# Optimization experiments

Hardware: AMD Instinct MI355X
Metric: run time of the kernel (lower is better)

Reference implementation:

```python
import jax, jax.numpy as jnp
import numpy as np

N = 8192        # nodes
V = 50000       # vocab = len(dict_node_names)
EMB = 256       # embedding_dim
XI = EMB // 2   # x_increased_dim = 128
DIN = EMB + XI  # 384, SelfAtt_ dim
H = 4           # n_heads
D = 128         # WGAT output_dim per head (fusion dim)
E = 131072      # edges
CHUNK = 32768   # chunk_size (E % CHUNK == 0)


def _ln(x, g, b, eps=1e-5):
    m = jnp.mean(x, axis=-1, keepdims=True)
    v = jnp.mean((x - m) ** 2, axis=-1, keepdims=True)
    return (x - m) * jax.lax.rsqrt(v + eps) * g + b


def _wgat(emb, src, dst, edge_attr, wi, bi, wj, bj, wt, bt, attn):
    # x_i = features at destination (aggregation target), x_j = source/neighbor
    x_i = emb[dst]                                   # [E, din]
    x_j = emb[src]                                   # [E, din]
    h = (x_i @ wi + bi).reshape(E, H, D) + (x_j @ wj + bj).reshape(E, H, D)
    a = jnp.einsum('ehd,hd->eh', h, attn)            # [E, H]
    a = a * edge_attr[:, None]                       # edge weights pre-softmax
    # faithful chunked softmax: normalize over edges WITHIN each chunk (dim=0 per chunk)
    a = jax.nn.softmax(a.reshape(E // CHUNK, CHUNK, H), axis=1).reshape(E, H)
    xt = (x_j @ wt + bt).reshape(E, H, D)            # [E, H, D]
    msg = jnp.einsum('ehd,eh->ed', xt, a)            # sum over heads -> [E, D]
    return jax.ops.segment_sum(msg, dst, num_segments=N)  # aggr='add'


def _emb_forward(ids, edge_index, x, edge_attr, embed,
                 qkv_w, qkv_b, proj_w, proj_b, fuse_w, fuse_b, ln1_g, ln1_b,
                 wi0, bi0, wj0, bj0, wt0, bt0, attn0, skip0_w, skip0_b,
                 wi1, bi1, wj1, bj1, wt1, bt1, attn1, skip1_w, skip1_b,
                 ln2_g, ln2_b):
    E_i = embed[ids]                                 # [N, EMB] gather
    z = jnp.concatenate([jnp.tile(x, (1, XI)), E_i], axis=-1)   # [N, DIN]
    # SelfAtt_ : full N x N attention over nodes, scale = DIN**-0.5
    qkv = z @ qkv_w + qkv_b
    q, k, v = jnp.split(qkv, 3, axis=-1)
    att = jax.nn.softmax((q @ k.T) * (DIN ** -0.5), axis=-1) @ v
    z = att @ proj_w + proj_b                        # [N, DIN]
    emb = jax.nn.silu(_ln(z @ fuse_w + fuse_b, ln1_g, ln1_b)) + E_i  # [N, EMB]
    src, dst = edge_index[0], edge_index[1]
    emb = _wgat(emb, src, dst, edge_attr, wi0, bi0, wj0, bj0, wt0, bt0, attn0)  # [N, D]
    s0 = emb @ skip0_w + skip0_b
    emb = _wgat(emb, src, dst, edge_attr, wi1, bi1, wj1, bj1, wt1, bt1, attn1)  # [N, D]
    s1 = emb @ skip1_w + skip1_b
    emb = _ln(emb + (s0 + s1) * 0.5, ln2_g, ln2_b)
    return emb


def setup_inputs() -> dict:
    key = jax.random.key(0)
    ks = jax.random.split(key, 32)

    def w(k, shape, scale=0.05):
        return jax.random.normal(k, shape, jnp.float32) * scale

    inp = {}
    inp['ids'] = jax.random.randint(ks[0], (N,), 0, V)
    inp['x'] = jax.random.normal(ks[1], (N, 1), jnp.float32)
    inp['edge_attr'] = jax.random.uniform(ks[2], (E,), jnp.float32)
    inp['edge_index'] = jax.random.randint(ks[3], (2, E), 0, N)
    inp['embed'] = w(ks[4], (V, EMB), 1.0)
    inp['qkv_w'] = w(ks[5], (DIN, 3 * DIN)); inp['qkv_b'] = jnp.zeros((3 * DIN,), jnp.float32)
    inp['proj_w'] = w(ks[6], (DIN, DIN));    inp['proj_b'] = jnp.zeros((DIN,), jnp.float32)
    inp['fuse_w'] = w(ks[7], (DIN, EMB));    inp['fuse_b'] = jnp.zeros((EMB,), jnp.float32)
    inp['ln1_g'] = jnp.ones((EMB,), jnp.float32); inp['ln1_b'] = jnp.zeros((EMB,), jnp.float32)
    # WGAT layer 0: in=EMB, out=D per head, H heads
    inp['wi0'] = w(ks[8], (EMB, H * D));  inp['bi0'] = jnp.zeros((H * D,), jnp.float32)
    inp['wj0'] = w(ks[9], (EMB, H * D));  inp['bj0'] = jnp.zeros((H * D,), jnp.float32)
    inp['wt0'] = w(ks[10], (EMB, H * D)); inp['bt0'] = jnp.zeros((H * D,), jnp.float32)
    inp['attn0'] = w(ks[11], (H, D), 0.1)
    inp['skip0_w'] = w(ks[12], (D, D));   inp['skip0_b'] = jnp.zeros((D,), jnp.float32)
    # WGAT layer 1: in=D
    inp['wi1'] = w(ks[13], (D, H * D));   inp['bi1'] = jnp.zeros((H * D,), jnp.float32)
    inp['wj1'] = w(ks[14], (D, H * D));   inp['bj1'] = jnp.zeros((H * D,), jnp.float32)
    inp['wt1'] = w(ks[15], (D, H * D));   inp['bt1'] = jnp.zeros((H * D,), jnp.float32)
    inp['attn1'] = w(ks[16], (H, D), 0.1)
    inp['skip1_w'] = w(ks[17], (D, D));   inp['skip1_b'] = jnp.zeros((D,), jnp.float32)
    inp['ln2_g'] = jnp.ones((D,), jnp.float32); inp['ln2_b'] = jnp.zeros((D,), jnp.float32)
    return inp


def reference(ids, x, edge_attr, edge_index, embed,
              qkv_w, qkv_b, proj_w, proj_b, fuse_w, fuse_b, ln1_g, ln1_b,
              wi0, bi0, wj0, bj0, wt0, bt0, attn0, skip0_w, skip0_b,
              wi1, bi1, wj1, bj1, wt1, bt1, attn1, skip1_w, skip1_b,
              ln2_g, ln2_b):
    emb = _emb_forward(ids, edge_index, x, edge_attr, embed,
                       qkv_w, qkv_b, proj_w, proj_b, fuse_w, fuse_b, ln1_g, ln1_b,
                       wi0, bi0, wj0, bj0, wt0, bt0, attn0, skip0_w, skip0_b,
                       wi1, bi1, wj1, bj1, wt1, bt1, attn1, skip1_w, skip1_b,
                       ln2_g, ln2_b)
    return (emb, embed, ids)
```

## Files before the change

### kernel.cpp

```cpp
#include <hip/hip_runtime.h>

typedef __attribute__((ext_vector_type(8))) short bfrag;
typedef __attribute__((ext_vector_type(4))) float f4;

#define MFMA(a,b,c) __builtin_amdgcn_mfma_f32_16x16x32_bf16(a,b,c,0,0,0)

__device__ __forceinline__ unsigned short f2b(float x){
  union { float f; unsigned int u; } v; v.f = x;
  unsigned int r = v.u + 0x7fffu + ((v.u >> 16) & 1u);
  return (unsigned short)(r >> 16);
}
__device__ __forceinline__ float b2f(unsigned short h){
  union { unsigned int u; float f; } v; v.u = ((unsigned int)h) << 16;
  return v.f;
}

__global__ __launch_bounds__(256) void k_prep(
    const float* __restrict__ qkv_w, const float* __restrict__ proj_w,
    const float* __restrict__ fuse_w, const float* __restrict__ wt0,
    const float* __restrict__ wt1, const float* __restrict__ sk0w,
    const float* __restrict__ wi0, const float* __restrict__ bi0,
    const float* __restrict__ wj0, const float* __restrict__ bj0,
    const float* __restrict__ wi1, const float* __restrict__ bi1,
    const float* __restrict__ wj1, const float* __restrict__ bj1,
    const float* __restrict__ attn0, const float* __restrict__ attn1,
    const float* __restrict__ bt0, const float* __restrict__ bt1,
    const float* __restrict__ sk0b,
    const float* __restrict__ embed, const int* __restrict__ ids,
    unsigned short* __restrict__ BtQKV, unsigned short* __restrict__ BtPROJ,
    unsigned short* __restrict__ BtFUSE, unsigned short* __restrict__ BtT0,
    unsigned short* __restrict__ BtT1,
    float* __restrict__ biasT0, float* __restrict__ biasT1,
    float* __restrict__ wsum, float* __restrict__ Ei)
{
  int b = blockIdx.x, t = threadIdx.x;
  if (b < 1152) {
    int idx = b*256 + t; int k = idx/1152, n = idx - k*1152;
    BtQKV[(size_t)n*256 + k] = f2b(qkv_w[128*1152 + idx]);
  } else if (b < 1728) {
    int idx = (b-1152)*256 + t; int k = idx/384, n = idx - k*384;
    BtPROJ[(size_t)n*384 + k] = f2b(proj_w[idx]);
  } else if (b < 2112) {
    int idx = (b-1728)*256 + t; int k = idx/256, n = idx - k*256;
    BtFUSE[(size_t)n*384 + k] = f2b(fuse_w[idx]);
  } else if (b < 2624) {
    int idx = (b-2112)*256 + t; int k = idx/512, n = idx - k*512;
    BtT0[(size_t)n*256 + k] = f2b(wt0[idx]);
  } else if (b < 2880) {
    int idx = (b-2624)*256 + t; int k = idx/512, n = idx - k*512;
    BtT1[(size_t)n*128 + k] = f2b(wt1[idx]);
  } else if (b < 2944) {
    int idx = (b-2880)*256 + t; int k = idx/128, n = idx - k*128;
    BtT1[(size_t)(512+n)*128 + k] = f2b(sk0w[idx]);
  } else if (b < 2948) {
    int idx = (b-2944)*256 + t;
    int h = idx >> 8, k = idx & 255;
    float s = 0.f;
    for (int d = 0; d < 128; ++d) s += wi0[(size_t)k*512 + h*128 + d] * attn0[h*128 + d];
    BtT0[(size_t)(512 + h)*256 + k] = f2b(s);
    if (idx < 4) {
      float sb = 0.f;
      for (int d = 0; d < 128; ++d) sb += bi0[idx*128 + d] * attn0[idx*128 + d];
      biasT0[512 + idx] = sb;
    }
  } else if (b < 2952) {
    int idx = (b-2948)*256 + t;
    int h = idx >> 8, k = idx & 255;
    float s = 0.f;
    for (int d = 0; d < 128; ++d) s += wj0[(size_t)k*512 + h*128 + d] * attn0[h*128 + d];
    BtT0[(size_t)(516 + h)*256 + k] = f2b(s);
    if (idx < 4) {
      float sb = 0.f;
      for (int d = 0; d < 128; ++d) sb += bj0[idx*128 + d] * attn0[idx*128 + d];
      biasT0[516 + idx] = sb;
    }
  } else if (b < 2954) {
    int idx = (b-2952)*256 + t;
    int h = idx >> 7, k = idx & 127;
    float s = 0.f;
    for (int d = 0; d < 128; ++d) s += wi1[(size_t)k*512 + h*128 + d] * attn1[h*128 + d];
    BtT1[(size_t)(640 + h)*128 + k] = f2b(s);
    if (idx < 4) {
      float sb = 0.f;
      for (int d = 0; d < 128; ++d) sb += bi1[idx*128 + d] * attn1[idx*128 + d];
      biasT1[640 + idx] = sb;
    }
  } else if (b < 2956) {
    int idx = (b-2954)*256 + t;
    int h = idx >> 7, k = idx & 127;
    float s = 0.f;
    for (int d = 0; d < 128; ++d) s += wj1[(size_t)k*512 + h*128 + d] * attn1[h*128 + d];
    BtT1[(size_t)(644 + h)*128 + k] = f2b(s);
    if (idx < 4) {
      float sb = 0.f;
      for (int d = 0; d < 128; ++d) sb += bj1[idx*128 + d] * attn1[idx*128 + d];
      biasT1[644 + idx] = sb;
    }
  } else if (b < 2958) {
    int idx = (b-2956)*256 + t; biasT0[idx] = bt0[idx];
  } else if (b < 2960) {
    int idx = (b-2958)*256 + t; biasT1[idx] = bt1[idx];
  } else if (b < 2961) {
    if (t < 128) biasT1[512 + t] = sk0b[t];
  } else if (b < 2966) {
    int n = (b-2961)*256 + t;
    if (n < 1152) {
      float s = 0.f;
      for (int k = 0; k < 128; ++k) s += qkv_w[(size_t)k*1152 + n];
      wsum[n] = s;
    }
  } else {
    int idx = (b-2966)*256 + t;
    int n = idx >> 6, c4 = idx & 63;
    reinterpret_cast<float4*>(Ei)[idx] =
        reinterpret_cast<const float4*>(embed + (size_t)ids[n]*256)[c4];
  }
}

__global__ void k_outcopy(const float* __restrict__ embed, const int* __restrict__ ids,
                          float* __restrict__ out){
  int i = blockIdx.x*256 + threadIdx.x;
  if (i < 3200000)
    reinterpret_cast<float4*>(out)[262144 + i] = reinterpret_cast<const float4*>(embed)[i];
  if (i < 8192) out[13848576 + i] = (float)ids[i];
}

__global__ void k_deg(const int* __restrict__ ei, int* __restrict__ deg){
  int e = blockIdx.x*256 + threadIdx.x; if (e >= 131072) return;
  atomicAdd(&deg[ei[131072 + e]], 1);
}

__global__ __launch_bounds__(1024) void k_scan(const int* __restrict__ deg,
                                               int* __restrict__ off, int* __restrict__ cursor){
  int t = threadIdx.x;
  int v[8]; int s = 0;
  #pragma unroll
  for (int i=0;i<8;++i){ v[i] = s; s += deg[t*8 + i]; }
  int lane = t & 63, w = t >> 6;
  int si = s;
  for (int o=1;o<64;o<<=1){ int u = __shfl_up(si, o); if (lane >= o) si += u; }
  __shared__ int wsum[16];
  if (lane == 63) wsum[w] = si;
  __syncthreads();
  if (t < 16) {
    int x = wsum[t];
    for (int o=1;o<16;o<<=1){ int u = __shfl_up(x, o); if (t >= o) x += u; }
    wsum[t] = x;
  }
  __syncthreads();
  int wbase = (w == 0) ? 0 : wsum[w-1];
  int base = wbase + (si - s);
  #pragma unroll
  for (int i=0;i<8;++i){ int o2 = base + v[i]; off[t*8+i] = o2; cursor[t*8+i] = o2; }
  if (t == 1023) off[8192] = wbase + si;
}

__global__ void k_fill(const int* __restrict__ ei, int* __restrict__ cursor,
                       int* __restrict__ elist){
  int e = blockIdx.x*256 + threadIdx.x; if (e >= 131072) return;
  int d = ei[131072 + e];
  int slot = atomicAdd(&cursor[d], 1);
  elist[slot] = e;
}

__global__ __launch_bounds__(256) void k_gemm(
    const float* __restrict__ A, int lda,
    const unsigned short* __restrict__ Bt, int K,
    const float* __restrict__ bias,
    float* __restrict__ C, int ldc, int mode,
    const float* __restrict__ xv, const float* __restrict__ wsum,
    unsigned short* __restrict__ qO, unsigned short* __restrict__ kO,
    unsigned short* __restrict__ vO)
{
  __shared__ unsigned short As[128*40];
  __shared__ unsigned short Bs[128*40];
  const int t = threadIdx.x;
  const int wid = t >> 6, l = t & 63;
  const int lr = l & 15, lg = l >> 4;
  const int arow0 = blockIdx.y*128, bn0 = blockIdx.x*128;
  const int wr = (wid >> 1)*64, wc = (wid & 1)*64;
  f4 zero = {0.f,0.f,0.f,0.f};
  f4 acc[4][4];
  #pragma unroll
  for (int i=0;i<4;++i)
    #pragma unroll
    for (int j=0;j<4;++j) acc[i][j] = zero;

  for (int k0 = 0; k0 < K; k0 += 32) {
    #pragma unroll
    for (int p=0;p<4;++p) {
      int row = p*32 + (t>>3);
      int c4  = (t&7)*4;
      float4 v = *reinterpret_cast<const float4*>(A + (size_t)(arow0+row)*lda + k0 + c4);
      ushort4 h4;
      h4.x = f2b(v.x); h4.y = f2b(v.y); h4.z = f2b(v.z); h4.w = f2b(v.w);
      *reinterpret_cast<ushort4*>(&As[row*40 + c4]) = h4;
    }
    #pragma unroll
    for (int p=0;p<2;++p) {
      int n  = p*64 + (t>>2);
      int c8 = (t&3)*8;
      int4 v = *reinterpret_cast<const int4*>(Bt + (size_t)(bn0+n)*K + k0 + c8);
      *reinterpret_cast<int4*>(&Bs[n*40 + c8]) = v;
    }
    __syncthreads();
    bfrag af[4], bfm[4];
    #pragma unroll
    for (int mi=0;mi<4;++mi) af[mi] = *reinterpret_cast<const bfrag*>(&As[(wr+mi*16+lr)*40 + lg*8]);
    #pragma unroll
    for (int ni=0;ni<4;++ni) bfm[ni] = *reinterpret_cast<const bfrag*>(&Bs[(wc+ni*16+lr)*40 + lg*8]);
    #pragma unroll
    for (int mi=0;mi<4;++mi)
      #pragma unroll
      for (int ni=0;ni<4;++ni)
        acc[mi][ni] = MFMA(af[mi], bfm[ni], acc[mi][ni]);
    __syncthreads();
  }
  #pragma unroll
  for (int mi=0;mi<4;++mi) {
    #pragma unroll
    for (int ni=0;ni<4;++ni) {
      int col = bn0 + wc + ni*16 + lr;
      float bv = bias[col];
      float wsv = (mode==1) ? wsum[col] : 0.f;
      #pragma unroll
      for (int i=0;i<4;++i) {
        int row = arow0 + wr + mi*16 + lg*4 + i;
        float val = acc[mi][ni][i] + bv;
        if (mode == 1) {
          val += xv[row]*wsv;
          if (col < 384) val *= 0.05103103631f;
          unsigned short hv = f2b(val);
          if (col < 384)      qO[(size_t)row*384 + col] = hv;
          else if (col < 768) kO[(size_t)row*384 + col - 384] = hv;
          else                vO[(size_t)(col-768)*8192 + row] = hv;
        } else {
          C[(size_t)row*ldc + col] = val;
        }
      }
    }
  }
}

__global__ __launch_bounds__(256,2) void k_flash(
    const unsigned short* __restrict__ qg,
    const unsigned short* __restrict__ kg,
    const unsigned short* __restrict__ vg,
    unsigned short* __restrict__ Opart, float* __restrict__ mpart, float* __restrict__ lpart)
{
  __shared__ unsigned short Ks[32*384];
  __shared__ unsigned short Vs[2][384*32];
  __shared__ unsigned short Ps[64*40];
  __shared__ float f_s[64];

  const int t = threadIdx.x;
  const int w = t >> 6, l = t & 63;
  const int lr = l & 15, lg = l >> 4;
  const int qbi = blockIdx.x >> 2, split = blockIdx.x & 3;
  const int qbase = qbi * 64;

  #define STAGE_K(JJ) do { \
    _Pragma("unroll") \
    for (int p_=0;p_<6;++p_) { \
      int idx_ = p_*256 + t; \
      int row_ = idx_ / 48, uu_ = idx_ - row_*48; \
      int ug_ = uu_ ^ (row_ & 7); \
      const unsigned short* gp_ = kg + (size_t)((JJ) + row_)*384 + ug_*8; \
      __builtin_amdgcn_global_load_lds((const __attribute__((address_space(1))) void*)gp_, \
          (__attribute__((address_space(3))) void*)&Ks[idx_*8], 16, 0, 0); \
    } } while(0)

  #define STAGE_V(JJ, BUF) do { \
    _Pragma("unroll") \
    for (int p_=0;p_<6;++p_) { \
      int idx_ = p_*256 + t; \
      int d_ = idx_ >> 2, u_ = idx_ & 3; \
      const unsigned short* gp_ = vg + (size_t)d_*8192 + (JJ) + u_*8; \
      __builtin_amdgcn_global_load_lds((const __attribute__((address_space(1))) void*)gp_, \
          (__attribute__((address_space(3))) void*)&Vs[BUF][idx_*8], 16, 0, 0); \
    } } while(0)

  bfrag qf[12];
  #pragma unroll
  for (int kk=0;kk<12;++kk)
    qf[kk] = *reinterpret_cast<const bfrag*>(qg + (size_t)(qbase + w*16 + lr)*384 + kk*32 + lg*8);

  f4 zero = {0.f,0.f,0.f,0.f};
  f4 o[4][6];
  #pragma unroll
  for (int a=0;a<4;++a)
    #pragma unroll
    for (int b=0;b<6;++b) o[a][b] = zero;

  float m = -3e38f, lsum = 0.f;
  const int j0beg = split*2048, jend = j0beg + 2048;

  STAGE_K(j0beg);
  STAGE_V(j0beg, 0);
  __syncthreads();
  int cur = 0;

  for (int j0 = j0beg; j0 < jend; j0 += 32) {
    f4 s0 = zero, s1 = zero;
    __builtin_amdgcn_s_setprio(1);
    #pragma unroll
    for (int kk=0;kk<12;++kk) {
      int su = ((kk*4 + lg) ^ (lr & 7)) * 8;
      bfrag k0 = *reinterpret_cast<const bfrag*>(&Ks[lr*384 + su]);
      bfrag k1 = *reinterpret_cast<const bfrag*>(&Ks[(16+lr)*384 + su]);
      s0 = MFMA(k0, qf[kk], s0);
      s1 = MFMA(k1, qf[kk], s1);
    }
    __builtin_amdgcn_s_setprio(0);

    float mt = fmaxf(fmaxf(fmaxf(s0[0],s0[1]),fmaxf(s0[2],s0[3])),
                     fmaxf(fmaxf(s1[0],s1[1]),fmaxf(s1[2],s1[3])));
    mt = fmaxf(mt, __shfl_xor(mt,16));
    mt = fmaxf(mt, __shfl_xor(mt,32));
    bool grew = mt > m;
    float mn = grew ? mt : m;
    float p0[4], p1[4];
    float sum = 0.f;
    #pragma unroll
    for (int i=0;i<4;++i) {
      p0[i] = __expf(s0[i]-mn); p1[i] = __expf(s1[i]-mn);
      sum += p0[i] + p1[i];
    }
    sum += __shfl_xor(sum,16);
    sum += __shfl_xor(sum,32);
    float f = 1.f;
    if (__any(grew)) {
      f = __expf(m - mn);
      lsum = lsum * f + sum;
      m = mn;
    } else {
      lsum += sum;
    }

    unsigned int pk0 = (unsigned int)f2b(p0[0]) | ((unsigned int)f2b(p0[1]) << 16);
    unsigned int pk1 = (unsigned int)f2b(p0[2]) | ((unsigned int)f2b(p0[3]) << 16);
    unsigned int pk2 = (unsigned int)f2b(p1[0]) | ((unsigned int)f2b(p1[1]) << 16);
    unsigned int pk3 = (unsigned int)f2b(p1[2]) | ((unsigned int)f2b(p1[3]) << 16);
    int prow = (w*16 + lr)*40;
    *reinterpret_cast<unsigned int*>(&Ps[prow + lg*4])          = pk0;
    *reinterpret_cast<unsigned int*>(&Ps[prow + lg*4 + 2])      = pk1;
    *reinterpret_cast<unsigned int*>(&Ps[prow + 16 + lg*4])     = pk2;
    *reinterpret_cast<unsigned int*>(&Ps[prow + 16 + lg*4 + 2]) = pk3;
    if (lg == 0) f_s[w*16 + lr] = f;

    __syncthreads();

    if (j0 + 32 < jend) { STAGE_K(j0 + 32); STAGE_V(j0 + 32, cur ^ 1); }

    bfrag pf[4], vf[6];
    #pragma unroll
    for (int qt=0;qt<4;++qt)
      pf[qt] = *reinterpret_cast<const bfrag*>(&Ps[(qt*16+lr)*40 + lg*8]);
    #pragma unroll
    for (int dt=0;dt<6;++dt)
      vf[dt] = *reinterpret_cast<const bfrag*>(&Vs[cur][(w*96 + dt*16 + lr)*32 + lg*8]);
    #pragma unroll
    for (int qt=0;qt<4;++qt) {
      #pragma unroll
      for (int i=0;i<4;++i) {
        float fr = f_s[qt*16 + lg*4 + i];
        #pragma unroll
        for (int dt=0;dt<6;++dt) o[qt][dt][i] *= fr;
      }
    }
    __builtin_amdgcn_s_setprio(1);
    #pragma unroll
    for (int qt=0;qt<4;++qt)
      #pragma unroll
      for (int dt=0;dt<6;++dt)
        o[qt][dt] = MFMA(pf[qt], vf[dt], o[qt][dt]);
    __builtin_amdgcn_s_setprio(0);

    __syncthreads();
    cur ^= 1;
  }
  #undef STAGE_K
  #undef STAGE_V

  unsigned short* Op = Opart + (size_t)split*8192*384;
  #pragma unroll
  for (int qt=0;qt<4;++qt)
    #pragma unroll
    for (int dt=0;dt<6;++dt)
      #pragma unroll
      for (int i=0;i<4;++i)
        Op[(size_t)(qbase + qt*16 + lg*4 + i)*384 + w*96 + dt*16 + lr] = f2b(o[qt][dt][i]);
  if (lg == 0) {
    mpart[split*8192 + qbase + w*16 + lr] = m;
    lpart[split*8192 + qbase + w*16 + lr] = lsum;
  }
}

__global__ void k_combine(const unsigned short* __restrict__ Op, const float* __restrict__ mp,
                          const float* __restrict__ lp, float* __restrict__ att)
{
  int gid = blockIdx.x*256 + threadIdx.x;
  int row = gid / 384;
  float m0 = mp[row], m1 = mp[8192+row], m2 = mp[16384+row], m3 = mp[24576+row];
  float M = fmaxf(fmaxf(m0,m1), fmaxf(m2,m3));
  float w0 = __expf(m0-M), w1 = __expf(m1-M), w2 = __expf(m2-M), w3 = __expf(m3-M);
  float L = lp[row]*w0 + lp[8192+row]*w1 + lp[16384+row]*w2 + lp[24576+row]*w3;
  const size_t Z = (size_t)8192*384;
  float acc = b2f(Op[gid])*w0 + b2f(Op[Z+gid])*w1 + b2f(Op[2*Z+gid])*w2 + b2f(Op[3*Z+gid])*w3;
  att[gid] = acc / L;
}

__global__ __launch_bounds__(256) void k_ln1(const float* __restrict__ pre, const float* __restrict__ Ei,
                      const float* __restrict__ g, const float* __restrict__ b,
                      float* __restrict__ out)
{
  int row = blockIdx.x, c = threadIdx.x;
  float v = pre[(size_t)row*256 + c];
  float s1 = v, s2 = v*v;
  #pragma unroll
  for (int o1=32;o1;o1>>=1){ s1 += __shfl_down(s1,o1); s2 += __shfl_down(s2,o1); }
  __shared__ float a1[4], a2[4];
  if ((c&63)==0){ a1[c>>6] = s1; a2[c>>6] = s2; }
  __syncthreads();
  float S1 = a1[0]+a1[1]+a1[2]+a1[3], S2 = a2[0]+a2[1]+a2[2]+a2[3];
  float mean = S1*(1.f/256.f), var = S2*(1.f/256.f) - mean*mean;
  float y = (v-mean)*rsqrtf(var+1e-5f)*g[c] + b[c];
  float sig = 1.f/(1.f+__expf(-y));
  out[(size_t)row*256 + c] = y*sig + Ei[(size_t)row*256 + c];
}

__global__ void k_escore(const int* __restrict__ ei, const float* __restrict__ ea,
                         const float* __restrict__ TC, int ldc, int aoff,
                         float* __restrict__ sc)
{
  int e = blockIdx.x*256 + threadIdx.x; if (e >= 131072) return;
  int s = ei[e], d = ei[131072 + e];
  float wv = ea[e];
  #pragma unroll
  for (int h=0; h<4; ++h) {
    float ai = TC[(size_t)d*ldc + aoff + h];
    float aj = TC[(size_t)s*ldc + aoff + 4 + h];
    sc[e*4 + h] = (ai + aj) * wv;
  }
}

__global__ __launch_bounds__(1024) void k_cstats(const float* __restrict__ sc,
                        float* __restrict__ mx, float* __restrict__ sm)
{
  int ch = blockIdx.x;
  int c = ch >> 2, h = ch & 3;
  int t = threadIdx.x;
  const float* base = sc + (size_t)c*131072 + h;
  float m = -3e38f;
  for (int i=t; i<32768; i+=1024) m = fmaxf(m, base[(size_t)i*4]);
  #pragma unroll
  for (int o1=32;o1;o1>>=1) m = fmaxf(m, __shfl_down(m,o1));
  __shared__ float red[16];
  if ((t&63)==0) red[t>>6] = m;
  __syncthreads();
  if (t == 0) { float x = red[0]; for (int i=1;i<16;++i) x = fmaxf(x, red[i]); red[0] = x; }
  __syncthreads();
  float M = red[0];
  float s = 0.f;
  for (int i=t; i<32768; i+=1024) s += __expf(base[(size_t)i*4] - M);
  #pragma unroll
  for (int o1=32;o1;o1>>=1) s += __shfl_down(s,o1);
  __shared__ float red2[16];
  if ((t&63)==0) red2[t>>6] = s;
  __syncthreads();
  if (t == 0) { float x = 0.f; for (int i=0;i<16;++i) x += red2[i]; mx[ch] = M; sm[ch] = x; }
}

__global__ void k_pnorm(float* __restrict__ sc, const float* __restrict__ mx,
                        const float* __restrict__ sm)
{
  int i = blockIdx.x*256 + threadIdx.x;
  int e = i >> 2, h = i & 3;
  int ch = (e >> 15)*4 + h;
  sc[i] = __expf(sc[i] - mx[ch]) / sm[ch];
}

__global__ __launch_bounds__(128) void k_aggr(const int* __restrict__ off,
                      const int* __restrict__ elist, const int* __restrict__ ei,
                      const float* __restrict__ sc,
                      const float* __restrict__ TC, int ldc, float* __restrict__ g)
{
  int n = blockIdx.x, d = threadIdx.x;
  int qb = off[n], qe = off[n+1];
  float acc = 0.f;
  for (int q = qb; q < qe; ++q) {
    int e = elist[q];
    int s = ei[e];
    float4 p = *reinterpret_cast<const float4*>(&sc[e*4]);
    const float* Tr = TC + (size_t)s*ldc;
    acc += p.x*Tr[d] + p.y*Tr[128+d] + p.z*Tr[256+d] + p.w*Tr[384+d];
  }
  g[(size_t)n*128 + d] = acc;
}

__global__ __launch_bounds__(128) void k_final(const float* __restrict__ g1, const float* __restrict__ TC1,
                       const float* __restrict__ sw, const float* __restrict__ sb,
                       const float* __restrict__ lg2, const float* __restrict__ lb2,
                       float* __restrict__ out)
{
  int row = blockIdx.x, c = threadIdx.x;
  __shared__ float gr[128];
  float gv = g1[(size_t)row*128 + c];
  gr[c] = gv; __syncthreads();
  float s1 = sb[c];
  #pragma unroll 8
  for (int k=0;k<128;++k) s1 += gr[k]*sw[k*128 + c];
  float s0 = TC1[(size_t)row*768 + 512 + c];
  float v = gv + 0.5f*(s0 + s1);
  float m1 = v, m2 = v*v;
  #pragma unroll
  for (int o1=32;o1;o1>>=1){ m1 += __shfl_down(m1,o1); m2 += __shfl_down(m2,o1); }
  __shared__ float a1[2], a2[2];
  if ((c&63)==0){ a1[c>>6]=m1; a2[c>>6]=m2; }
  __syncthreads();
  float S1 = a1[0]+a1[1], S2 = a2[0]+a2[1];
  float mean = S1*(1.f/128.f), var = S2*(1.f/128.f) - mean*mean;
  out[(size_t)row*128 + c] = (v-mean)*rsqrtf(var+1e-5f)*lg2[c] + lb2[c];
}

extern "C" void kernel_launch(void* const* d_in, const int* in_sizes, int n_in,
                              void* d_out, int out_size, void* d_ws, size_t ws_size,
                              hipStream_t stream)
{
  const int*   ids    = (const int*)  d_in[0];
  const float* x      = (const float*)d_in[1];
  const float* ea     = (const float*)d_in[2];
  const int*   eidx   = (const int*)  d_in[3];
  const float* embed  = (const float*)d_in[4];
  const float* qkv_w  = (const float*)d_in[5];
  const float* qkv_b  = (const float*)d_in[6];
  const float* proj_w = (const float*)d_in[7];
  const float* proj_b = (const float*)d_in[8];
  const float* fuse_w = (const float*)d_in[9];
  const float* fuse_b = (const float*)d_in[10];
  const float* ln1_g  = (const float*)d_in[11];
  const float* ln1_b  = (const float*)d_in[12];
  const float* wi0 = (const float*)d_in[13]; const float* bi0 = (const float*)d_in[14];
  const float* wj0 = (const float*)d_in[15]; const float* bj0 = (const float*)d_in[16];
  const float* wt0 = (const float*)d_in[17]; const float* bt0 = (const float*)d_in[18];
  const float* attn0 = (const float*)d_in[19];
  const float* sk0w = (const float*)d_in[20]; const float* sk0b = (const float*)d_in[21];
  const float* wi1 = (const float*)d_in[22]; const float* bi1 = (const float*)d_in[23];
  const float* wj1 = (const float*)d_in[24]; const float* bj1 = (const float*)d_in[25];
  const float* wt1 = (const float*)d_in[26]; const float* bt1 = (const float*)d_in[27];
  const float* attn1 = (const float*)d_in[28];
  const float* sk1w = (const float*)d_in[29]; const float* sk1b = (const float*)d_in[30];
  const float* ln2_g = (const float*)d_in[31]; const float* ln2_b = (const float*)d_in[32];

  char* ws = (char*)d_ws;
  const size_t MBy = (size_t)1 << 20;

  unsigned short* BtQKV  = (unsigned short*)(ws + 0);
  unsigned short* BtPROJ = (unsigned short*)(ws + 589824);
  unsigned short* BtFUSE = (unsigned short*)(ws + 884736);
  unsigned short* BtT0   = (unsigned short*)(ws + 1081344);
  unsigned short* BtT1   = (unsigned short*)(ws + 1409024);
  float* biasT0 = (float*)(ws + 1605632);
  float* biasT1 = (float*)(ws + 1608192);
  float* wsum   = (float*)(ws + 1611264);
  float* mxb    = (float*)(ws + 1615872);
  float* smb    = (float*)(ws + 1615936);
  int* deg    = (int*)(ws + 1703936);
  int* cursor = (int*)(ws + 1736704);
  int* off    = (int*)(ws + 1769472);

  float* Ei   = (float*)(ws + 2*MBy);
  unsigned short* qb = (unsigned short*)(ws + 10*MBy);
  unsigned short* kb = (unsigned short*)(ws + 17*MBy);
  unsigned short* vb = (unsigned short*)(ws + 24*MBy);
  float* att  = (float*)(ws + 31*MBy);
  float* z2   = (float*)(ws + 10*MBy);
  float* pre  = (float*)(ws + 45*MBy);
  float* emb0 = (float*)(ws + 31*MBy);
  float* TC0  = (float*)(ws + 43*MBy);
  float* sc0  = (float*)(ws + 26*MBy);
  float* g0   = (float*)(ws + 2*MBy);
  float* TC1  = (float*)(ws + 6*MBy);
  float* sc1  = (float*)(ws + 43*MBy);
  float* g1   = (float*)(ws + 47448064);
  int* elist  = (int*)(ws + 64*MBy);

  float* out = (float*)d_out;
  unsigned short* Opart = (unsigned short*)d_out;
  float* mpart = out + 6815744;
  float* lpart = out + 6848512;

  hipMemsetAsync(ws, 0, 2*MBy, stream);

  k_prep<<<5014, 256, 0, stream>>>(qkv_w, proj_w, fuse_w, wt0, wt1, sk0w,
                                   wi0, bi0, wj0, bj0, wi1, bi1, wj1, bj1,
                                   attn0, attn1, bt0, bt1, sk0b, embed, ids,
                                   BtQKV, BtPROJ, BtFUSE, BtT0, BtT1,
                                   biasT0, biasT1, wsum, Ei);
  k_deg<<<512, 256, 0, stream>>>(eidx, deg);
  k_scan<<<1, 1024, 0, stream>>>(deg, off, cursor);
  k_fill<<<512, 256, 0, stream>>>(eidx, cursor, elist);

  k_gemm<<<dim3(9,64), 256, 0, stream>>>(Ei, 256, BtQKV, 256, qkv_b, nullptr, 0, 1,
                                         x, wsum, qb, kb, vb);
  k_flash<<<512, 256, 0, stream>>>(qb, kb, vb, Opart, mpart, lpart);
  k_combine<<<12288, 256, 0, stream>>>(Opart, mpart, lpart, att);
  k_outcopy<<<12500, 256, 0, stream>>>(embed, ids, out);

  k_gemm<<<dim3(3,64), 256, 0, stream>>>(att, 384, BtPROJ, 384, proj_b, z2, 384, 0,
                                         nullptr, nullptr, nullptr, nullptr, nullptr);
  k_gemm<<<dim3(2,64), 256, 0, stream>>>(z2, 384, BtFUSE, 384, fuse_b, pre, 256, 0,
                                         nullptr, nullptr, nullptr, nullptr, nullptr);
  k_ln1<<<8192, 256, 0, stream>>>(pre, Ei, ln1_g, ln1_b, emb0);

  k_gemm<<<dim3(5,64), 256, 0, stream>>>(emb0, 256, BtT0, 256, biasT0, TC0, 640, 0,
                                         nullptr, nullptr, nullptr, nullptr, nullptr);
  k_escore<<<512, 256, 0, stream>>>(eidx, ea, TC0, 640, 512, sc0);
  k_cstats<<<16, 1024, 0, stream>>>(sc0, mxb, smb);
  k_pnorm<<<2048, 256, 0, stream>>>(sc0, mxb, smb);
  k_aggr<<<8192, 128, 0, stream>>>(off, elist, eidx, sc0, TC0, 640, g0);

  k_gemm<<<dim3(6,64), 256, 0, stream>>>(g0, 128, BtT1, 128, biasT1, TC1, 768, 0,
                                         nullptr, nullptr, nullptr, nullptr, nullptr);
  k_escore<<<512, 256, 0, stream>>>(eidx, ea, TC1, 768, 640, sc1);
  k_cstats<<<16, 1024, 0, stream>>>(sc1, mxb, smb);
  k_pnorm<<<2048, 256, 0, stream>>>(sc1, mxb, smb);
  k_aggr<<<8192, 128, 0, stream>>>(off, elist, eidx, sc1, TC1, 768, g1);

  k_final<<<8192, 128, 0, stream>>>(g1, TC1, sk1w, sk1b, ln2_g, ln2_b, out);
}
```

Baseline: 474.8 us.

## Fold proj into fuse weights, fuse split-K combine into GEMM, lazy flash rescale

After: 531.3 us. 11.9% more time.

```diff
diff --git a/kernel.cpp b/kernel.cpp
--- a/kernel.cpp
+++ b/kernel.cpp
@@ -17,7 +17,9 @@
 
 __global__ __launch_bounds__(256) void k_prep(
     const float* __restrict__ qkv_w, const float* __restrict__ proj_w,
-    const float* __restrict__ fuse_w, const float* __restrict__ wt0,
+    const float* __restrict__ proj_b, const float* __restrict__ fuse_w,
+    const float* __restrict__ fuse_b,
+    const float* __restrict__ wt0,
     const float* __restrict__ wt1, const float* __restrict__ sk0w,
     const float* __restrict__ wi0, const float* __restrict__ bi0,
     const float* __restrict__ wj0, const float* __restrict__ bj0,
@@ -27,9 +29,9 @@
     const float* __restrict__ bt0, const float* __restrict__ bt1,
     const float* __restrict__ sk0b,
     const float* __restrict__ embed, const int* __restrict__ ids,
-    unsigned short* __restrict__ BtQKV, unsigned short* __restrict__ BtPROJ,
-    unsigned short* __restrict__ BtFUSE, unsigned short* __restrict__ BtT0,
-    unsigned short* __restrict__ BtT1,
+    unsigned short* __restrict__ BtQKV, unsigned short* __restrict__ BtW2,
+    unsigned short* __restrict__ BtT0, unsigned short* __restrict__ BtT1,
+    float* __restrict__ biasW2,
     float* __restrict__ biasT0, float* __restrict__ biasT1,
     float* __restrict__ wsum, float* __restrict__ Ei)
 {
@@ -37,23 +39,26 @@
   if (b < 1152) {
     int idx = b*256 + t; int k = idx/1152, n = idx - k*1152;
     BtQKV[(size_t)n*256 + k] = f2b(qkv_w[128*1152 + idx]);
-  } else if (b < 1728) {
-    int idx = (b-1152)*256 + t; int k = idx/384, n = idx - k*384;
-    BtPROJ[(size_t)n*384 + k] = f2b(proj_w[idx]);
-  } else if (b < 2112) {
-    int idx = (b-1728)*256 + t; int k = idx/256, n = idx - k*256;
-    BtFUSE[(size_t)n*384 + k] = f2b(fuse_w[idx]);
-  } else if (b < 2624) {
-    int idx = (b-2112)*256 + t; int k = idx/512, n = idx - k*512;
+  } else if (b < 1536) {
+    int k = b - 1152;
+    float s = 0.f;
+    for (int j = 0; j < 384; ++j) s += proj_w[(size_t)k*384 + j] * fuse_w[(size_t)j*256 + t];
+    BtW2[(size_t)t*384 + k] = f2b(s);
+  } else if (b == 1536) {
+    float s = fuse_b[t];
+    for (int j = 0; j < 384; ++j) s += proj_b[j] * fuse_w[(size_t)j*256 + t];
+    biasW2[t] = s;
+  } else if (b < 2049) {
+    int idx = (b-1537)*256 + t; int k = idx/512, n = idx - k*512;
     BtT0[(size_t)n*256 + k] = f2b(wt0[idx]);
-  } else if (b < 2880) {
-    int idx = (b-2624)*256 + t; int k = idx/512, n = idx - k*512;
+  } else if (b < 2305) {
+    int idx = (b-2049)*256 + t; int k = idx/512, n = idx - k*512;
     BtT1[(size_t)n*128 + k] = f2b(wt1[idx]);
-  } else if (b < 2944) {
-    int idx = (b-2880)*256 + t; int k = idx/128, n = idx - k*128;
+  } else if (b < 2369) {
+    int idx = (b-2305)*256 + t; int k = idx/128, n = idx - k*128;
     BtT1[(size_t)(512+n)*128 + k] = f2b(sk0w[idx]);
-  } else if (b < 2948) {
-    int idx = (b-2944)*256 + t;
+  } else if (b < 2373) {
+    int idx = (b-2369)*256 + t;
     int h = idx >> 8, k = idx & 255;
     float s = 0.f;
     for (int d = 0; d < 128; ++d) s += wi0[(size_t)k*512 + h*128 + d] * attn0[h*128 + d];
@@ -63,8 +68,8 @@
       for (int d = 0; d < 128; ++d) sb += bi0[idx*128 + d] * attn0[idx*128 + d];
       biasT0[512 + idx] = sb;
     }
-  } else if (b < 2952) {
-    int idx = (b-2948)*256 + t;
+  } else if (b < 2377) {
+    int idx = (b-2373)*256 + t;
     int h = idx >> 8, k = idx & 255;
     float s = 0.f;
     for (int d = 0; d < 128; ++d) s += wj0[(size_t)k*512 + h*128 + d] * attn0[h*128 + d];
@@ -74,8 +79,8 @@
       for (int d = 0; d < 128; ++d) sb += bj0[idx*128 + d] * attn0[idx*128 + d];
       biasT0[516 + idx] = sb;
     }
-  } else if (b < 2954) {
-    int idx = (b-2952)*256 + t;
+  } else if (b < 2379) {
+    int idx = (b-2377)*256 + t;
     int h = idx >> 7, k = idx & 127;
     float s = 0.f;
     for (int d = 0; d < 128; ++d) s += wi1[(size_t)k*512 + h*128 + d] * attn1[h*128 + d];
@@ -85,8 +90,8 @@
       for (int d = 0; d < 128; ++d) sb += bi1[idx*128 + d] * attn1[idx*128 + d];
       biasT1[640 + idx] = sb;
     }
-  } else if (b < 2956) {
-    int idx = (b-2954)*256 + t;
+  } else if (b < 2381) {
+    int idx = (b-2379)*256 + t;
     int h = idx >> 7, k = idx & 127;
     float s = 0.f;
     for (int d = 0; d < 128; ++d) s += wj1[(size_t)k*512 + h*128 + d] * attn1[h*128 + d];
@@ -96,21 +101,21 @@
       for (int d = 0; d < 128; ++d) sb += bj1[idx*128 + d] * attn1[idx*128 + d];
       biasT1[644 + idx] = sb;
     }
-  } else if (b < 2958) {
-    int idx = (b-2956)*256 + t; biasT0[idx] = bt0[idx];
-  } else if (b < 2960) {
-    int idx = (b-2958)*256 + t; biasT1[idx] = bt1[idx];
-  } else if (b < 2961) {
+  } else if (b < 2383) {
+    int idx = (b-2381)*256 + t; biasT0[idx] = bt0[idx];
+  } else if (b < 2385) {
+    int idx = (b-2383)*256 + t; biasT1[idx] = bt1[idx];
+  } else if (b == 2385) {
     if (t < 128) biasT1[512 + t] = sk0b[t];
-  } else if (b < 2966) {
-    int n = (b-2961)*256 + t;
+  } else if (b < 2391) {
+    int n = (b-2386)*256 + t;
     if (n < 1152) {
       float s = 0.f;
       for (int k = 0; k < 128; ++k) s += qkv_w[(size_t)k*1152 + n];
       wsum[n] = s;
     }
   } else {
-    int idx = (b-2966)*256 + t;
+    int idx = (b-2391)*256 + t;
     int n = idx >> 6, c4 = idx & 63;
     reinterpret_cast<float4*>(Ei)[idx] =
         reinterpret_cast<const float4*>(embed + (size_t)ids[n]*256)[c4];
@@ -170,7 +175,8 @@
     float* __restrict__ C, int ldc, int mode,
     const float* __restrict__ xv, const float* __restrict__ wsum,
     unsigned short* __restrict__ qO, unsigned short* __restrict__ kO,
-    unsigned short* __restrict__ vO)
+    unsigned short* __restrict__ vO,
+    const unsigned short* __restrict__ opA, const float* __restrict__ cw)
 {
   __shared__ unsigned short As[128*40];
   __shared__ unsigned short Bs[128*40];
@@ -191,9 +197,22 @@
     for (int p=0;p<4;++p) {
       int row = p*32 + (t>>3);
       int c4  = (t&7)*4;
-      float4 v = *reinterpret_cast<const float4*>(A + (size_t)(arow0+row)*lda + k0 + c4);
       ushort4 h4;
-      h4.x = f2b(v.x); h4.y = f2b(v.y); h4.z = f2b(v.z); h4.w = f2b(v.w);
+      if (mode == 2) {
+        const float* w4 = &cw[(arow0+row)*4];
+        float a0=0.f,a1=0.f,a2=0.f,a3=0.f;
+        #pragma unroll
+        for (int s=0;s<4;++s) {
+          ushort4 u = *reinterpret_cast<const ushort4*>(
+              opA + (size_t)s*3145728 + (size_t)(arow0+row)*384 + k0 + c4);
+          float wv = w4[s];
+          a0 += b2f(u.x)*wv; a1 += b2f(u.y)*wv; a2 += b2f(u.z)*wv; a3 += b2f(u.w)*wv;
+        }
+        h4.x = f2b(a0); h4.y = f2b(a1); h4.z = f2b(a2); h4.w = f2b(a3);
+      } else {
+        float4 v = *reinterpret_cast<const float4*>(A + (size_t)(arow0+row)*lda + k0 + c4);
+        h4.x = f2b(v.x); h4.y = f2b(v.y); h4.z = f2b(v.z); h4.w = f2b(v.w);
+      }
       *reinterpret_cast<ushort4*>(&As[row*40 + c4]) = h4;
     }
     #pragma unroll
@@ -317,8 +336,9 @@
                      fmaxf(fmaxf(s1[0],s1[1]),fmaxf(s1[2],s1[3])));
     mt = fmaxf(mt, __shfl_xor(mt,16));
     mt = fmaxf(mt, __shfl_xor(mt,32));
-    bool grew = mt > m;
-    float mn = grew ? mt : m;
+    bool need = mt > m + 8.f;
+    bool doresc = __any(need);
+    float mn = doresc ? fmaxf(m, mt) : m;
     float p0[4], p1[4];
     float sum = 0.f;
     #pragma unroll
@@ -329,7 +349,7 @@
     sum += __shfl_xor(sum,16);
     sum += __shfl_xor(sum,32);
     float f = 1.f;
-    if (__any(grew)) {
+    if (doresc) {
       f = __expf(m - mn);
       lsum = lsum * f + sum;
       m = mn;
@@ -359,14 +379,23 @@
     #pragma unroll
     for (int dt=0;dt<6;++dt)
       vf[dt] = *reinterpret_cast<const bfrag*>(&Vs[cur][(w*96 + dt*16 + lr)*32 + lg*8]);
+
+    f4 fr[4];
+    bool anyr = false;
     #pragma unroll
     for (int qt=0;qt<4;++qt) {
+      fr[qt] = *reinterpret_cast<const f4*>(&f_s[qt*16 + lg*4]);
+      anyr = anyr || (fr[qt][0]!=1.f) || (fr[qt][1]!=1.f) || (fr[qt][2]!=1.f) || (fr[qt][3]!=1.f);
+    }
+    if (__any(anyr)) {
       #pragma unroll
-      for (int i=0;i<4;++i) {
-        float fr = f_s[qt*16 + lg*4 + i];
+      for (int qt=0;qt<4;++qt)
         #pragma unroll
-        for (int dt=0;dt<6;++dt) o[qt][dt][i] *= fr;
-      }
+        for (int i=0;i<4;++i) {
+          float frv = fr[qt][i];
+          #pragma unroll
+          for (int dt=0;dt<6;++dt) o[qt][dt][i] *= frv;
+        }
     }
     __builtin_amdgcn_s_setprio(1);
     #pragma unroll
@@ -396,18 +425,17 @@
   }
 }
 
-__global__ void k_combine(const unsigned short* __restrict__ Op, const float* __restrict__ mp,
-                          const float* __restrict__ lp, float* __restrict__ att)
-{
-  int gid = blockIdx.x*256 + threadIdx.x;
-  int row = gid / 384;
-  float m0 = mp[row], m1 = mp[8192+row], m2 = mp[16384+row], m3 = mp[24576+row];
+__global__ void k_cw(const float* __restrict__ mp, const float* __restrict__ lp,
+                     float* __restrict__ cw)
+{
+  int r = blockIdx.x*256 + threadIdx.x;
+  float m0 = mp[r], m1 = mp[8192+r], m2 = mp[16384+r], m3 = mp[24576+r];
   float M = fmaxf(fmaxf(m0,m1), fmaxf(m2,m3));
   float w0 = __expf(m0-M), w1 = __expf(m1-M), w2 = __expf(m2-M), w3 = __expf(m3-M);
-  float L = lp[row]*w0 + lp[8192+row]*w1 + lp[16384+row]*w2 + lp[24576+row]*w3;
-  const size_t Z = (size_t)8192*384;
-  float acc = b2f(Op[gid])*w0 + b2f(Op[Z+gid])*w1 + b2f(Op[2*Z+gid])*w2 + b2f(Op[3*Z+gid])*w3;
-  att[gid] = acc / L;
+  float L = lp[r]*w0 + lp[8192+r]*w1 + lp[16384+r]*w2 + lp[24576+r]*w3;
+  float inv = 1.f / L;
+  float4 o4 = make_float4(w0*inv, w1*inv, w2*inv, w3*inv);
+  *reinterpret_cast<float4*>(&cw[r*4]) = o4;
 }
 
 __global__ __launch_bounds__(256) void k_ln1(const float* __restrict__ pre, const float* __restrict__ Ei,
@@ -451,24 +479,31 @@
   int c = ch >> 2, h = ch & 3;
   int t = threadIdx.x;
   const float* base = sc + (size_t)c*131072 + h;
-  float m = -3e38f;
-  for (int i=t; i<32768; i+=1024) m = fmaxf(m, base[(size_t)i*4]);
-  #pragma unroll
-  for (int o1=32;o1;o1>>=1) m = fmaxf(m, __shfl_down(m,o1));
-  __shared__ float red[16];
-  if ((t&63)==0) red[t>>6] = m;
+  float lm = -3e38f, ls = 0.f;
+  for (int i=t; i<32768; i+=1024) {
+    float v = base[(size_t)i*4];
+    if (v > lm) { ls = ls*__expf(lm - v) + 1.f; lm = v; }
+    else        ls += __expf(v - lm);
+  }
+  #pragma unroll
+  for (int o1=32;o1;o1>>=1) {
+    float om = __shfl_down(lm,o1), os = __shfl_down(ls,o1);
+    float M2 = fmaxf(lm, om);
+    ls = ls*__expf(lm-M2) + os*__expf(om-M2);
+    lm = M2;
+  }
+  __shared__ float rm[16], rs[16];
+  if ((t&63)==0){ rm[t>>6] = lm; rs[t>>6] = ls; }
   __syncthreads();
-  if (t == 0) { float x = red[0]; for (int i=1;i<16;++i) x = fmaxf(x, red[i]); red[0] = x; }
-  __syncthreads();
-  float M = red[0];
-  float s = 0.f;
-  for (int i=t; i<32768; i+=1024) s += __expf(base[(size_t)i*4] - M);
-  #pragma unroll
-  for (int o1=32;o1;o1>>=1) s += __shfl_down(s,o1);
-  __shared__ float red2[16];
-  if ((t&63)==0) red2[t>>6] = s;
-  __syncthreads();
-  if (t == 0) { float x = 0.f; for (int i=0;i<16;++i) x += red2[i]; mx[ch] = M; sm[ch] = x; }
+  if (t == 0) {
+    float M = rm[0], S = rs[0];
+    for (int i=1;i<16;++i) {
+      float M2 = fmaxf(M, rm[i]);
+      S = S*__expf(M-M2) + rs[i]*__expf(rm[i]-M2);
+      M = M2;
+    }
+    mx[ch] = M; sm[ch] = S;
+  }
 }
 
 __global__ void k_pnorm(float* __restrict__ sc, const float* __restrict__ mx,
@@ -556,8 +591,8 @@
   const size_t MBy = (size_t)1 << 20;
 
   unsigned short* BtQKV  = (unsigned short*)(ws + 0);
-  unsigned short* BtPROJ = (unsigned short*)(ws + 589824);
-  unsigned short* BtFUSE = (unsigned short*)(ws + 884736);
+  unsigned short* BtW2   = (unsigned short*)(ws + 589824);
+  float* biasW2 = (float*)(ws + 884736);
   unsigned short* BtT0   = (unsigned short*)(ws + 1081344);
   unsigned short* BtT1   = (unsigned short*)(ws + 1409024);
   float* biasT0 = (float*)(ws + 1605632);
@@ -568,13 +603,12 @@
   int* deg    = (int*)(ws + 1703936);
   int* cursor = (int*)(ws + 1736704);
   int* off    = (int*)(ws + 1769472);
+  float* cw   = (float*)(ws + 1806336);
 
   float* Ei   = (float*)(ws + 2*MBy);
   unsigned short* qb = (unsigned short*)(ws + 10*MBy);
   unsigned short* kb = (unsigned short*)(ws + 17*MBy);
   unsigned short* vb = (unsigned short*)(ws + 24*MBy);
-  float* att  = (float*)(ws + 31*MBy);
-  float* z2   = (float*)(ws + 10*MBy);
   float* pre  = (float*)(ws + 45*MBy);
   float* emb0 = (float*)(ws + 31*MBy);
   float* TC0  = (float*)(ws + 43*MBy);
@@ -592,36 +626,38 @@
 
   hipMemsetAsync(ws, 0, 2*MBy, stream);
 
-  k_prep<<<5014, 256, 0, stream>>>(qkv_w, proj_w, fuse_w, wt0, wt1, sk0w,
+  k_prep<<<4439, 256, 0, stream>>>(qkv_w, proj_w, proj_b, fuse_w, fuse_b,
+                                   wt0, wt1, sk0w,
                                    wi0, bi0, wj0, bj0, wi1, bi1, wj1, bj1,
                                    attn0, attn1, bt0, bt1, sk0b, embed, ids,
-                                   BtQKV, BtPROJ, BtFUSE, BtT0, BtT1,
-                                   biasT0, biasT1, wsum, Ei);
+                                   BtQKV, BtW2, BtT0, BtT1,
+                                   biasW2, biasT0, biasT1, wsum, Ei);
   k_deg<<<512, 256, 0, stream>>>(eidx, deg);
   k_scan<<<1, 1024, 0, stream>>>(deg, off, cursor);
   k_fill<<<512, 256, 0, stream>>>(eidx, cursor, elist);
 
   k_gemm<<<dim3(9,64), 256, 0, stream>>>(Ei, 256, BtQKV, 256, qkv_b, nullptr, 0, 1,
-                                         x, wsum, qb, kb, vb);
+                                         x, wsum, qb, kb, vb, nullptr, nullptr);
   k_flash<<<512, 256, 0, stream>>>(qb, kb, vb, Opart, mpart, lpart);
-  k_combine<<<12288, 256, 0, stream>>>(Opart, mpart, lpart, att);
+  k_cw<<<32, 256, 0, stream>>>(mpart, lpart, cw);
+
+  k_gemm<<<dim3(2,64), 256, 0, stream>>>(nullptr, 0, BtW2, 384, biasW2, pre, 256, 2,
+                                         nullptr, nullptr, nullptr, nullptr, nullptr,
+                                         Opart, cw);
   k_outcopy<<<12500, 256, 0, stream>>>(embed, ids, out);
-
-  k_gemm<<<dim3(3,64), 256, 0, stream>>>(att, 384, BtPROJ, 384, proj_b, z2, 384, 0,
-                                         nullptr, nullptr, nullptr, nullptr, nullptr);
-  k_gemm<<<dim3(2,64), 256, 0, stream>>>(z2, 384, BtFUSE, 384, fuse_b, pre, 256, 0,
-                                         nullptr, nullptr, nullptr, nullptr, nullptr);
   k_ln1<<<8192, 256, 0, stream>>>(pre, Ei, ln1_g, ln1_b, emb0);
 
   k_gemm<<<dim3(5,64), 256, 0, stream>>>(emb0, 256, BtT0, 256, biasT0, TC0, 640, 0,
-                                         nullptr, nullptr, nullptr, nullptr, nullptr);
+                                         nullptr, nullptr, nullptr, nullptr, nullptr,
+                                         nullptr, nullptr);
   k_escore<<<512, 256, 0, stream>>>(eidx, ea, TC0, 640, 512, sc0);
   k_cstats<<<16, 1024, 0, stream>>>(sc0, mxb, smb);
   k_pnorm<<<2048, 256, 0, stream>>>(sc0, mxb, smb);
   k_aggr<<<8192, 128, 0, stream>>>(off, elist, eidx, sc0, TC0, 640, g0);
 
   k_gemm<<<dim3(6,64), 256, 0, stream>>>(g0, 128, BtT1, 128, biasT1, TC1, 768, 0,
-                                         nullptr, nullptr, nullptr, nullptr, nullptr);
+                                         nullptr, nullptr, nullptr, nullptr, nullptr,
+                                         nullptr, nullptr);
   k_escore<<<512, 256, 0, stream>>>(eidx, ea, TC1, 768, 640, sc1);
   k_cstats<<<16, 1024, 0, stream>>>(sc1, mxb, smb);
   k_pnorm<<<2048, 256, 0, stream>>>(sc1, mxb, smb);
```
